# Kernel optimization log

Hardware: AMD Instinct MI355X
Metric: run time of the kernel (lower is better)

## Reference

```python
import jax, jax.numpy as jnp
import numpy as np

N_HEADS = 16
D_EMBED = 1024
D_HEAD = D_EMBED // N_HEADS  # 64
B, S = 2, 2048


def setup_inputs() -> dict:
    key = jax.random.key(0)
    ks = jax.random.split(key, 6)
    k = jax.random.normal(ks[0], (B, S, D_EMBED), dtype=jnp.float32)
    q = jax.random.normal(ks[1], (B, S, D_EMBED), dtype=jnp.float32)
    v = jax.random.normal(ks[2], (B, S, D_EMBED), dtype=jnp.float32)
    # per-head projections, shared across heads (nn.Linear(d_head, d_head, bias=False))
    scale = 1.0 / np.sqrt(D_HEAD)
    Wk = jax.random.normal(ks[3], (D_HEAD, D_HEAD), dtype=jnp.float32) * scale
    Wq = jax.random.normal(ks[4], (D_HEAD, D_HEAD), dtype=jnp.float32) * scale
    Wv = jax.random.normal(ks[5], (D_HEAD, D_HEAD), dtype=jnp.float32) * scale
    return {"k": k, "q": q, "v": v, "Wk": Wk, "Wq": Wq, "Wv": Wv}


def reference(k, q, v, Wk, Wq, Wv):
    b, s, _ = k.shape
    # split heads: [b, s, h, dh]
    kh = k.reshape(b, s, N_HEADS, D_HEAD)
    qh = q.reshape(b, s, N_HEADS, D_HEAD)
    vh = v.reshape(b, s, N_HEADS, D_HEAD)
    # shared per-head linear projection (y = x @ W^T, torch Linear convention)
    kh = jnp.einsum('bshd,ed->bshe', kh, Wk)
    qh = jnp.einsum('bshd,ed->bshe', qh, Wq)
    vh = jnp.einsum('bshd,ed->bshe', vh, Wv)
    # attention scores [b, h, q, k]
    scores = jnp.einsum('bqhd,bkhd->bhqk', qh, kh) / np.sqrt(D_HEAD).astype(np.float32)
    attn = jax.nn.softmax(scores, axis=-1)
    out = jnp.einsum('bhqk,bkhd->bqhd', attn, vh)
    return out.reshape(b, s, D_EMBED)
```

## Files before the change

kernel.cpp:

```cpp
#include <hip/hip_runtime.h>
#include <hip/hip_bf16.h>

typedef unsigned short u16;
typedef __bf16 bf16x8 __attribute__((ext_vector_type(8)));
typedef float f32x4 __attribute__((ext_vector_type(4)));

#define S_LEN 2048
#define NH 16
#define NB 2
#define HEAD_ELEMS (NB * NH * S_LEN * 64)

#if __has_builtin(__builtin_amdgcn_exp2f)
#define EXP2(x) __builtin_amdgcn_exp2f(x)
#else
#define EXP2(x) exp2f(x)
#endif

#define QSCALE 0.180336880f
#define SHIFT2 30.0f

__device__ __forceinline__ bf16x8 pack8(float4 a, float4 b, float sc) {
    union { bf16x8 v; __hip_bfloat162 h[4]; } r;
    r.h[0] = __float22bfloat162_rn(make_float2(a.x * sc, a.y * sc));
    r.h[1] = __float22bfloat162_rn(make_float2(a.z * sc, a.w * sc));
    r.h[2] = __float22bfloat162_rn(make_float2(b.x * sc, b.y * sc));
    r.h[3] = __float22bfloat162_rn(make_float2(b.z * sc, b.w * sc));
    return r.v;
}

__global__ __launch_bounds__(256) void proj_kq(
    const float* __restrict__ kin, const float* __restrict__ qin,
    const float* __restrict__ Wk, const float* __restrict__ Wq,
    u16* __restrict__ Kh, u16* __restrict__ Qh)
{
    __shared__ __align__(16) u16 Yld[8 * 16 * 72];

    const int tid = threadIdx.x;
    const int wave = tid >> 6;
    const int lane = tid & 63;
    const int quad = lane >> 4;
    const int l15 = lane & 15;
    const int stile = blockIdx.x;
    const int p = blockIdx.y;
    const int hh = blockIdx.z;
    const long row0 = (long)stile * 16;
    const int b = (int)(row0 >> 11);
    const int s0 = (int)(row0 & 2047);

    const float* X = p ? qin : kin;
    const float* W = p ? Wq : Wk;
    const float sc = p ? QSCALE : 1.0f;

    const float* xr0 = X + (row0 + l15) * 1024 + (hh * 8 + wave * 2) * 64 + quad * 8;
    const float* xr1 = xr0 + 64;
    float4 xa[4], xb[4];
    xa[0] = *(const float4*)(xr0);      xa[1] = *(const float4*)(xr0 + 4);
    xa[2] = *(const float4*)(xr0 + 32); xa[3] = *(const float4*)(xr0 + 36);
    xb[0] = *(const float4*)(xr1);      xb[1] = *(const float4*)(xr1 + 4);
    xb[2] = *(const float4*)(xr1 + 32); xb[3] = *(const float4*)(xr1 + 36);

    bf16x8 wf[4][2];
    #pragma unroll
    for (int nt = 0; nt < 4; ++nt) {
        const float* wr = W + (nt * 16 + l15) * 64 + quad * 8;
        wf[nt][0] = pack8(*(const float4*)(wr),      *(const float4*)(wr + 4),  sc);
        wf[nt][1] = pack8(*(const float4*)(wr + 32), *(const float4*)(wr + 36), sc);
    }

    #pragma unroll
    for (int hp = 0; hp < 2; ++hp) {
        const int hl = wave * 2 + hp;
        bf16x8 a0 = pack8(hp ? xb[0] : xa[0], hp ? xb[1] : xa[1], 1.0f);
        bf16x8 a1 = pack8(hp ? xb[2] : xa[2], hp ? xb[3] : xa[3], 1.0f);
        #pragma unroll
        for (int nt = 0; nt < 4; ++nt) {
            f32x4 c = (f32x4){0.f, 0.f, 0.f, 0.f};
            c = __builtin_amdgcn_mfma_f32_16x16x32_bf16(a0, wf[nt][0], c, 0, 0, 0);
            c = __builtin_amdgcn_mfma_f32_16x16x32_bf16(a1, wf[nt][1], c, 0, 0, 0);
            union { __hip_bfloat162 h2; u16 u[2]; } x01, x23;
            x01.h2 = __float22bfloat162_rn(make_float2(c[0], c[1]));
            x23.h2 = __float22bfloat162_rn(make_float2(c[2], c[3]));
            int base = (hl * 16 + quad * 4) * 72 + nt * 16 + l15;
            Yld[base]       = x01.u[0];
            Yld[base + 72]  = x01.u[1];
            Yld[base + 144] = x23.u[0];
            Yld[base + 216] = x23.u[1];
        }
    }
    __syncthreads();

    u16* dst = p ? Qh : Kh;
    #pragma unroll
    for (int it = 0; it < 4; ++it) {
        int idx = tid + it * 256;
        int eg = idx & 7, s = (idx >> 3) & 15, hl = idx >> 7;
        int bh = b * NH + hh * 8 + hl;
        *(float4*)(dst + ((long)bh * S_LEN + s0 + s) * 64 + eg * 8) =
            *(const float4*)&Yld[(hl * 16 + s) * 72 + eg * 8];
    }
}

__global__ __launch_bounds__(256) void proj_v(
    const float* __restrict__ vin, const float* __restrict__ Wv, u16* __restrict__ Vt)
{
    __shared__ __align__(16) u16 Vtile[64 * 72];

    const int tid = threadIdx.x;
    const int wave = tid >> 6;
    const int lane = tid & 63;
    const int quad = lane >> 4;
    const int l15 = lane & 15;
    const long row0 = (long)blockIdx.x * 64;
    const int b = (int)(row0 >> 11);
    const int s0 = (int)(row0 & 2047);
    const int h = blockIdx.y;
    const int bh = b * NH + h;

    const float* xr = vin + (row0 + wave * 16 + l15) * 1024 + h * 64 + quad * 8;
    float4 x4[4];
    x4[0] = *(const float4*)(xr);      x4[1] = *(const float4*)(xr + 4);
    x4[2] = *(const float4*)(xr + 32); x4[3] = *(const float4*)(xr + 36);

    bf16x8 wf[4][2];
    #pragma unroll
    for (int dt = 0; dt < 4; ++dt) {
        const float* wr = Wv + (dt * 16 + l15) * 64 + quad * 8;
        wf[dt][0] = pack8(*(const float4*)(wr),      *(const float4*)(wr + 4),  1.0f);
        wf[dt][1] = pack8(*(const float4*)(wr + 32), *(const float4*)(wr + 36), 1.0f);
    }

    bf16x8 x0 = pack8(x4[0], x4[1], 1.0f);
    bf16x8 x1 = pack8(x4[2], x4[3], 1.0f);

    #pragma unroll
    for (int dt = 0; dt < 4; ++dt) {
        f32x4 c = (f32x4){0.f, 0.f, 0.f, 0.f};
        c = __builtin_amdgcn_mfma_f32_16x16x32_bf16(wf[dt][0], x0, c, 0, 0, 0);
        c = __builtin_amdgcn_mfma_f32_16x16x32_bf16(wf[dt][1], x1, c, 0, 0, 0);
        int base = (dt * 16 + quad * 4) * 72 + wave * 16 + l15;
        union { __hip_bfloat162 h2; u16 u[2]; } x01, x23;
        x01.h2 = __float22bfloat162_rn(make_float2(c[0], c[1]));
        x23.h2 = __float22bfloat162_rn(make_float2(c[2], c[3]));
        Vtile[base]       = x01.u[0];
        Vtile[base + 72]  = x01.u[1];
        Vtile[base + 144] = x23.u[0];
        Vtile[base + 216] = x23.u[1];
    }
    __syncthreads();

    u16* dst = Vt + (long)bh * 64 * S_LEN + s0;
    #pragma unroll
    for (int it = 0; it < 2; ++it) {
        int idx = tid + it * 256;
        int sg = idx & 7, e = idx >> 3;
        *(float4*)(dst + (long)e * S_LEN + sg * 8) = *(const float4*)&Vtile[e * 72 + sg * 8];
    }
}

__global__ __launch_bounds__(256, 2) void attn_kernel(
    const u16* __restrict__ Qh, const u16* __restrict__ Kh,
    const u16* __restrict__ Vt, float* __restrict__ out)
{
    __shared__ __align__(16) u16 Qld[64 * 72];
    __shared__ __align__(16) float Old[4][64 * 20];
    __shared__ float lbc[4][64];

    const int tid = threadIdx.x;
    const int wave = tid >> 6;
    const int lane = tid & 63;
    const int quad = lane >> 4;
    const int l15 = lane & 15;
    const int qb = blockIdx.x;
    const int bh = blockIdx.y;
    const int b = bh >> 4, h = bh & 15;
    const int q0 = qb * 64;
    const u16* kb = Kh + (long)bh * S_LEN * 64;
    const u16* vb = Vt + (long)bh * 64 * S_LEN;

    {
        const u16* qp = Qh + ((long)bh * S_LEN + q0) * 64;
        #pragma unroll
        for (int i = 0; i < 2; ++i) {
            int idx = tid + i * 256;
            int row = idx >> 3, gg = idx & 7;
            *(float4*)&Qld[row * 72 + gg * 8] = *(const float4*)(qp + row * 64 + gg * 8);
        }
    }
    __syncthreads();

    const int krow_off = ((l15 >> 2) * 8 + (l15 & 3)) * 64;

    f32x4 oacc[4][4];
    #pragma unroll
    for (int g = 0; g < 4; ++g)
        #pragma unroll
        for (int dt = 0; dt < 4; ++dt) oacc[g][dt] = (f32x4){0.f, 0.f, 0.f, 0.f};
    float rs[4] = {0.f, 0.f, 0.f, 0.f};

    for (int kt = wave; kt < S_LEN / 64; kt += 4) {
        const u16* kt_p = kb + (long)kt * 4096;
        const u16* vt_p = vb + kt * 64;
        #pragma unroll
        for (int c = 0; c < 2; ++c) {
            bf16x8 kf[2][2], vf[4];
            #pragma unroll
            for (int nn = 0; nn < 2; ++nn) {
                const u16* kr = kt_p + c * 2048 + krow_off + nn * 256 + quad * 8;
                kf[nn][0] = *(const bf16x8*)(kr);
                kf[nn][1] = *(const bf16x8*)(kr + 32);
            }
            #pragma unroll
            for (int dt = 0; dt < 4; ++dt)
                vf[dt] = *(const bf16x8*)(vt_p + (long)(dt * 16 + l15) * S_LEN + c * 32 + quad * 8);

            #pragma unroll
            for (int g = 0; g < 4; ++g) {
                const u16* qrow = &Qld[(g * 16 + l15) * 72 + quad * 8];
                bf16x8 qb0 = *(const bf16x8*)(qrow);
                bf16x8 qb1 = *(const bf16x8*)(qrow + 32);
                f32x4 s0 = (f32x4){0.f, 0.f, 0.f, 0.f};
                f32x4 s1 = (f32x4){0.f, 0.f, 0.f, 0.f};
                s0 = __builtin_amdgcn_mfma_f32_16x16x32_bf16(kf[0][0], qb0, s0, 0, 0, 0);
                s0 = __builtin_amdgcn_mfma_f32_16x16x32_bf16(kf[0][1], qb1, s0, 0, 0, 0);
                s1 = __builtin_amdgcn_mfma_f32_16x16x32_bf16(kf[1][0], qb0, s1, 0, 0, 0);
                s1 = __builtin_amdgcn_mfma_f32_16x16x32_bf16(kf[1][1], qb1, s1, 0, 0, 0);

                float p00 = EXP2(s0[0] - SHIFT2), p01 = EXP2(s0[1] - SHIFT2);
                float p02 = EXP2(s0[2] - SHIFT2), p03 = EXP2(s0[3] - SHIFT2);
                float p10 = EXP2(s1[0] - SHIFT2), p11 = EXP2(s1[1] - SHIFT2);
                float p12 = EXP2(s1[2] - SHIFT2), p13 = EXP2(s1[3] - SHIFT2);
                rs[g] += ((p00 + p01) + (p02 + p03)) + ((p10 + p11) + (p12 + p13));

                union { bf16x8 v; __hip_bfloat162 h2[4]; } pf;
                pf.h2[0] = __float22bfloat162_rn(make_float2(p00, p01));
                pf.h2[1] = __float22bfloat162_rn(make_float2(p02, p03));
                pf.h2[2] = __float22bfloat162_rn(make_float2(p10, p11));
                pf.h2[3] = __float22bfloat162_rn(make_float2(p12, p13));

                #pragma unroll
                for (int dt = 0; dt < 4; ++dt)
                    oacc[g][dt] = __builtin_amdgcn_mfma_f32_16x16x32_bf16(vf[dt], pf.v, oacc[g][dt], 0, 0, 0);
            }
        }
    }

    #pragma unroll
    for (int g = 0; g < 4; ++g) {
        rs[g] += __shfl_xor(rs[g], 16);
        rs[g] += __shfl_xor(rs[g], 32);
    }
    if (lane < 16) {
        #pragma unroll
        for (int g = 0; g < 4; ++g) lbc[wave][g * 16 + lane] = rs[g];
    }
    __syncthreads();

    const int rq = tid >> 2, seg = tid & 3;
    const float linv = 1.0f / (lbc[0][rq] + lbc[1][rq] + lbc[2][rq] + lbc[3][rq]);
    float* op = out + ((long)(b * S_LEN + q0 + rq)) * 1024 + h * 64;

    #pragma unroll
    for (int ph = 0; ph < 4; ++ph) {
        #pragma unroll
        for (int g = 0; g < 4; ++g)
            *(f32x4*)&Old[wave][(g * 16 + l15) * 20 + quad * 4] = oacc[g][ph];
        __syncthreads();
        f32x4 a = (f32x4){0.f, 0.f, 0.f, 0.f};
        #pragma unroll
        for (int w = 0; w < 4; ++w) a += *(const f32x4*)&Old[w][rq * 20 + seg * 4];
        *(float4*)(op + ph * 16 + seg * 4) =
            make_float4(a[0] * linv, a[1] * linv, a[2] * linv, a[3] * linv);
        __syncthreads();
    }
}

extern "C" void kernel_launch(void* const* d_in, const int* in_sizes, int n_in,
                              void* d_out, int out_size, void* d_ws, size_t ws_size,
                              hipStream_t stream) {
    const float* kin = (const float*)d_in[0];
    const float* qin = (const float*)d_in[1];
    const float* vin = (const float*)d_in[2];
    const float* Wk  = (const float*)d_in[3];
    const float* Wq  = (const float*)d_in[4];
    const float* Wv  = (const float*)d_in[5];
    float* out = (float*)d_out;

    u16* wsp = (u16*)d_ws;
    u16* Kh = wsp;
    u16* Qh = wsp + (long)HEAD_ELEMS;
    u16* Vt = wsp + 2 * (long)HEAD_ELEMS;

    dim3 kqg(256, 2, 2);
    proj_kq<<<kqg, 256, 0, stream>>>(kin, qin, Wk, Wq, Kh, Qh);
    dim3 vg(64, 16);
    proj_v<<<vg, 256, 0, stream>>>(vin, Wv, Vt);
    dim3 g(S_LEN / 64, NB * NH);
    attn_kernel<<<g, 256, 0, stream>>>(Qh, Kh, Vt, out);
}
```

Baseline: 177.2 us.

## Keep Q in registers and double-buffer K/V register loads with MFMA priority

Q fragments now load straight from global memory into registers instead of being staged through shared memory, which removes the LDS tile and a block barrier. The K/V loop becomes a software pipeline with two register buffers, so the next half-tile's global loads are issued before computing on the current one, hiding load latency. The score shift is folded into the MFMA accumulator's initial value, and s_setprio raises wave priority around the MFMA sections. The cost is higher register pressure from holding Q and two K/V buffers, which could spill or limit occupancy under launch_bounds(256,2). The last iteration issues a redundant reload of the final tile.

```diff
diff --git a/kernel.cpp b/kernel.cpp
--- a/kernel.cpp
+++ b/kernel.cpp
@@ -161,12 +161,11 @@
     const u16* __restrict__ Qh, const u16* __restrict__ Kh,
     const u16* __restrict__ Vt, float* __restrict__ out)
 {
-    __shared__ __align__(16) u16 Qld[64 * 72];
     __shared__ __align__(16) float Old[4][64 * 20];
     __shared__ float lbc[4][64];
 
     const int tid = threadIdx.x;
-    const int wave = tid >> 6;
+    const int wave = __builtin_amdgcn_readfirstlane(tid >> 6);
     const int lane = tid & 63;
     const int quad = lane >> 4;
     const int l15 = lane & 15;
@@ -177,18 +176,18 @@
     const u16* kb = Kh + (long)bh * S_LEN * 64;
     const u16* vb = Vt + (long)bh * 64 * S_LEN;
 
+    const int koff = ((l15 >> 2) * 8 + (l15 & 3)) * 64 + quad * 8;
+    const int voff = l15 * S_LEN + quad * 8;
+
+    bf16x8 qf[4][2];
     {
-        const u16* qp = Qh + ((long)bh * S_LEN + q0) * 64;
-        #pragma unroll
-        for (int i = 0; i < 2; ++i) {
-            int idx = tid + i * 256;
-            int row = idx >> 3, gg = idx & 7;
-            *(float4*)&Qld[row * 72 + gg * 8] = *(const float4*)(qp + row * 64 + gg * 8);
+        const u16* qp = Qh + ((long)bh * S_LEN + q0 + l15) * 64 + quad * 8;
+        #pragma unroll
+        for (int g = 0; g < 4; ++g) {
+            qf[g][0] = *(const bf16x8*)(qp + g * 16 * 64);
+            qf[g][1] = *(const bf16x8*)(qp + g * 16 * 64 + 32);
         }
     }
-    __syncthreads();
-
-    const int krow_off = ((l15 >> 2) * 8 + (l15 & 3)) * 64;
 
     f32x4 oacc[4][4];
     #pragma unroll
@@ -197,51 +196,65 @@
         for (int dt = 0; dt < 4; ++dt) oacc[g][dt] = (f32x4){0.f, 0.f, 0.f, 0.f};
     float rs[4] = {0.f, 0.f, 0.f, 0.f};
 
-    for (int kt = wave; kt < S_LEN / 64; kt += 4) {
-        const u16* kt_p = kb + (long)kt * 4096;
-        const u16* vt_p = vb + kt * 64;
-        #pragma unroll
-        for (int c = 0; c < 2; ++c) {
-            bf16x8 kf[2][2], vf[4];
-            #pragma unroll
-            for (int nn = 0; nn < 2; ++nn) {
-                const u16* kr = kt_p + c * 2048 + krow_off + nn * 256 + quad * 8;
-                kf[nn][0] = *(const bf16x8*)(kr);
-                kf[nn][1] = *(const bf16x8*)(kr + 32);
-            }
+    auto loadKV = [&](const u16* kp, const u16* vp,
+                      bf16x8 (&kf)[2][2], bf16x8 (&vf)[4]) {
+        #pragma unroll
+        for (int nn = 0; nn < 2; ++nn) {
+            const u16* kr = kp + koff + nn * 256;
+            kf[nn][0] = *(const bf16x8*)(kr);
+            kf[nn][1] = *(const bf16x8*)(kr + 32);
+        }
+        #pragma unroll
+        for (int dt = 0; dt < 4; ++dt)
+            vf[dt] = *(const bf16x8*)(vp + voff + dt * 16 * S_LEN);
+    };
+
+    auto compute = [&](const bf16x8 (&kf)[2][2], const bf16x8 (&vf)[4]) {
+        #pragma unroll
+        for (int g = 0; g < 4; ++g) {
+            f32x4 s0 = (f32x4){-SHIFT2, -SHIFT2, -SHIFT2, -SHIFT2};
+            f32x4 s1 = (f32x4){-SHIFT2, -SHIFT2, -SHIFT2, -SHIFT2};
+            __builtin_amdgcn_s_setprio(1);
+            s0 = __builtin_amdgcn_mfma_f32_16x16x32_bf16(kf[0][0], qf[g][0], s0, 0, 0, 0);
+            s0 = __builtin_amdgcn_mfma_f32_16x16x32_bf16(kf[0][1], qf[g][1], s0, 0, 0, 0);
+            s1 = __builtin_amdgcn_mfma_f32_16x16x32_bf16(kf[1][0], qf[g][0], s1, 0, 0, 0);
+            s1 = __builtin_amdgcn_mfma_f32_16x16x32_bf16(kf[1][1], qf[g][1], s1, 0, 0, 0);
+            __builtin_amdgcn_s_setprio(0);
+
+            float p00 = EXP2(s0[0]), p01 = EXP2(s0[1]);
+            float p02 = EXP2(s0[2]), p03 = EXP2(s0[3]);
+            float p10 = EXP2(s1[0]), p11 = EXP2(s1[1]);
+            float p12 = EXP2(s1[2]), p13 = EXP2(s1[3]);
+            rs[g] += ((p00 + p01) + (p02 + p03)) + ((p10 + p11) + (p12 + p13));
+
+            union { bf16x8 v; __hip_bfloat162 h2[4]; } pf;
+            pf.h2[0] = __float22bfloat162_rn(make_float2(p00, p01));
+            pf.h2[1] = __float22bfloat162_rn(make_float2(p02, p03));
+            pf.h2[2] = __float22bfloat162_rn(make_float2(p10, p11));
+            pf.h2[3] = __float22bfloat162_rn(make_float2(p12, p13));
+
+            __builtin_amdgcn_s_setprio(1);
             #pragma unroll
             for (int dt = 0; dt < 4; ++dt)
-                vf[dt] = *(const bf16x8*)(vt_p + (long)(dt * 16 + l15) * S_LEN + c * 32 + quad * 8);
-
-            #pragma unroll
-            for (int g = 0; g < 4; ++g) {
-                const u16* qrow = &Qld[(g * 16 + l15) * 72 + quad * 8];
-                bf16x8 qb0 = *(const bf16x8*)(qrow);
-                bf16x8 qb1 = *(const bf16x8*)(qrow + 32);
-                f32x4 s0 = (f32x4){0.f, 0.f, 0.f, 0.f};
-                f32x4 s1 = (f32x4){0.f, 0.f, 0.f, 0.f};
-                s0 = __builtin_amdgcn_mfma_f32_16x16x32_bf16(kf[0][0], qb0, s0, 0, 0, 0);
-                s0 = __builtin_amdgcn_mfma_f32_16x16x32_bf16(kf[0][1], qb1, s0, 0, 0, 0);
-                s1 = __builtin_amdgcn_mfma_f32_16x16x32_bf16(kf[1][0], qb0, s1, 0, 0, 0);
-                s1 = __builtin_amdgcn_mfma_f32_16x16x32_bf16(kf[1][1], qb1, s1, 0, 0, 0);
-
-                float p00 = EXP2(s0[0] - SHIFT2), p01 = EXP2(s0[1] - SHIFT2);
-                float p02 = EXP2(s0[2] - SHIFT2), p03 = EXP2(s0[3] - SHIFT2);
-                float p10 = EXP2(s1[0] - SHIFT2), p11 = EXP2(s1[1] - SHIFT2);
-                float p12 = EXP2(s1[2] - SHIFT2), p13 = EXP2(s1[3] - SHIFT2);
-                rs[g] += ((p00 + p01) + (p02 + p03)) + ((p10 + p11) + (p12 + p13));
-
-                union { bf16x8 v; __hip_bfloat162 h2[4]; } pf;
-                pf.h2[0] = __float22bfloat162_rn(make_float2(p00, p01));
-                pf.h2[1] = __float22bfloat162_rn(make_float2(p02, p03));
-                pf.h2[2] = __float22bfloat162_rn(make_float2(p10, p11));
-                pf.h2[3] = __float22bfloat162_rn(make_float2(p12, p13));
-
-                #pragma unroll
-                for (int dt = 0; dt < 4; ++dt)
-                    oacc[g][dt] = __builtin_amdgcn_mfma_f32_16x16x32_bf16(vf[dt], pf.v, oacc[g][dt], 0, 0, 0);
-            }
+                oacc[g][dt] = __builtin_amdgcn_mfma_f32_16x16x32_bf16(vf[dt], pf.v, oacc[g][dt], 0, 0, 0);
+            __builtin_amdgcn_s_setprio(0);
         }
+    };
+
+    bf16x8 kfA[2][2], vfA[4], kfB[2][2], vfB[4];
+    const u16* kp = kb + wave * 4096;
+    const u16* vp = vb + wave * 64;
+    loadKV(kp, vp, kfA, vfA);
+
+    #pragma unroll 1
+    for (int kt = wave; kt < S_LEN / 64; kt += 4) {
+        loadKV(kp + 2048, vp + 32, kfB, vfB);
+        compute(kfA, vfA);
+        const u16* nkp = (kt < S_LEN / 64 - 4) ? kp + 4 * 4096 : kp;
+        const u16* nvp = (kt < S_LEN / 64 - 4) ? vp + 4 * 64   : vp;
+        loadKV(nkp, nvp, kfA, vfA);
+        compute(kfB, vfB);
+        kp = nkp; vp = nvp;
     }
 
     #pragma unroll
```

Measured after the change: 182.5 us. +3.0%, slower.

## Fuse K/Q/V projections into one launch and pre-swizzle K/V into fragment order

Applied to the files above, without the earlier changes.

Merges the KQ and V projection kernels into a single 2048-block launch. It also writes K and V into the workspace in MFMA-fragment order, so each lane in the attention kernel loads its bf16x8 fragments with fully contiguous 16-byte accesses instead of strided row gathers. This is meant to cut one launch and make the attention kernel's K/V global loads coalesced. The cost is more complex index arithmetic in the projection stores and a layout shared across kernels that is harder to maintain.

```diff
diff --git a/kernel.cpp b/kernel.cpp
--- a/kernel.cpp
+++ b/kernel.cpp
@@ -9,6 +9,7 @@
 #define NH 16
 #define NB 2
 #define HEAD_ELEMS (NB * NH * S_LEN * 64)
+#define BH_ELEMS (S_LEN * 64)
 
 #if __has_builtin(__builtin_amdgcn_exp2f)
 #define EXP2(x) __builtin_amdgcn_exp2f(x)
@@ -28,10 +29,12 @@
     return r.v;
 }
 
-__global__ __launch_bounds__(256) void proj_kq(
+__global__ __launch_bounds__(256) void proj_fused(
     const float* __restrict__ kin, const float* __restrict__ qin,
+    const float* __restrict__ vin,
     const float* __restrict__ Wk, const float* __restrict__ Wq,
-    u16* __restrict__ Kh, u16* __restrict__ Qh)
+    const float* __restrict__ Wv,
+    u16* __restrict__ Kh, u16* __restrict__ Qh, u16* __restrict__ Vt)
 {
     __shared__ __align__(16) u16 Yld[8 * 16 * 72];
 
@@ -40,120 +43,134 @@
     const int lane = tid & 63;
     const int quad = lane >> 4;
     const int l15 = lane & 15;
-    const int stile = blockIdx.x;
-    const int p = blockIdx.y;
-    const int hh = blockIdx.z;
-    const long row0 = (long)stile * 16;
-    const int b = (int)(row0 >> 11);
-    const int s0 = (int)(row0 & 2047);
-
-    const float* X = p ? qin : kin;
-    const float* W = p ? Wq : Wk;
-    const float sc = p ? QSCALE : 1.0f;
-
-    const float* xr0 = X + (row0 + l15) * 1024 + (hh * 8 + wave * 2) * 64 + quad * 8;
-    const float* xr1 = xr0 + 64;
-    float4 xa[4], xb[4];
-    xa[0] = *(const float4*)(xr0);      xa[1] = *(const float4*)(xr0 + 4);
-    xa[2] = *(const float4*)(xr0 + 32); xa[3] = *(const float4*)(xr0 + 36);
-    xb[0] = *(const float4*)(xr1);      xb[1] = *(const float4*)(xr1 + 4);
-    xb[2] = *(const float4*)(xr1 + 32); xb[3] = *(const float4*)(xr1 + 36);
-
-    bf16x8 wf[4][2];
-    #pragma unroll
-    for (int nt = 0; nt < 4; ++nt) {
-        const float* wr = W + (nt * 16 + l15) * 64 + quad * 8;
-        wf[nt][0] = pack8(*(const float4*)(wr),      *(const float4*)(wr + 4),  sc);
-        wf[nt][1] = pack8(*(const float4*)(wr + 32), *(const float4*)(wr + 36), sc);
-    }
-
-    #pragma unroll
-    for (int hp = 0; hp < 2; ++hp) {
-        const int hl = wave * 2 + hp;
-        bf16x8 a0 = pack8(hp ? xb[0] : xa[0], hp ? xb[1] : xa[1], 1.0f);
-        bf16x8 a1 = pack8(hp ? xb[2] : xa[2], hp ? xb[3] : xa[3], 1.0f);
+    const int bid = blockIdx.x;
+
+    if (bid < 1024) {
+        const int stile = bid & 255;
+        const int p = (bid >> 8) & 1;
+        const int hh = bid >> 9;
+        const long row0 = (long)stile * 16;
+        const int b = (int)(row0 >> 11);
+        const int s0 = (int)(row0 & 2047);
+
+        const float* X = p ? qin : kin;
+        const float* W = p ? Wq : Wk;
+        const float sc = p ? QSCALE : 1.0f;
+
+        const float* xr0 = X + (row0 + l15) * 1024 + (hh * 8 + wave * 2) * 64 + quad * 8;
+        const float* xr1 = xr0 + 64;
+        float4 xa[4], xb[4];
+        xa[0] = *(const float4*)(xr0);      xa[1] = *(const float4*)(xr0 + 4);
+        xa[2] = *(const float4*)(xr0 + 32); xa[3] = *(const float4*)(xr0 + 36);
+        xb[0] = *(const float4*)(xr1);      xb[1] = *(const float4*)(xr1 + 4);
+        xb[2] = *(const float4*)(xr1 + 32); xb[3] = *(const float4*)(xr1 + 36);
+
+        bf16x8 wf[4][2];
         #pragma unroll
         for (int nt = 0; nt < 4; ++nt) {
+            const float* wr = W + (nt * 16 + l15) * 64 + quad * 8;
+            wf[nt][0] = pack8(*(const float4*)(wr),      *(const float4*)(wr + 4),  sc);
+            wf[nt][1] = pack8(*(const float4*)(wr + 32), *(const float4*)(wr + 36), sc);
+        }
+
+        #pragma unroll
+        for (int hp = 0; hp < 2; ++hp) {
+            const int hl = wave * 2 + hp;
+            bf16x8 a0 = pack8(hp ? xb[0] : xa[0], hp ? xb[1] : xa[1], 1.0f);
+            bf16x8 a1 = pack8(hp ? xb[2] : xa[2], hp ? xb[3] : xa[3], 1.0f);
+            #pragma unroll
+            for (int nt = 0; nt < 4; ++nt) {
+                f32x4 c = (f32x4){0.f, 0.f, 0.f, 0.f};
+                c = __builtin_amdgcn_mfma_f32_16x16x32_bf16(a0, wf[nt][0], c, 0, 0, 0);
+                c = __builtin_amdgcn_mfma_f32_16x16x32_bf16(a1, wf[nt][1], c, 0, 0, 0);
+                union { __hip_bfloat162 h2; u16 u[2]; } x01, x23;
+                x01.h2 = __float22bfloat162_rn(make_float2(c[0], c[1]));
+                x23.h2 = __float22bfloat162_rn(make_float2(c[2], c[3]));
+                int base = (hl * 16 + quad * 4) * 72 + nt * 16 + l15;
+                Yld[base]       = x01.u[0];
+                Yld[base + 72]  = x01.u[1];
+                Yld[base + 144] = x23.u[0];
+                Yld[base + 216] = x23.u[1];
+            }
+        }
+        __syncthreads();
+
+        if (p) {
+            #pragma unroll
+            for (int it = 0; it < 4; ++it) {
+                int idx = tid + it * 256;
+                int eg = idx & 7, s = (idx >> 3) & 15, hl = idx >> 7;
+                int bh = b * NH + hh * 8 + hl;
+                *(float4*)(Qh + ((long)bh * S_LEN + s0 + s) * 64 + eg * 8) =
+                    *(const float4*)&Yld[(hl * 16 + s) * 72 + eg * 8];
+            }
+        } else {
+            #pragma unroll
+            for (int it = 0; it < 4; ++it) {
+                int idx = tid + it * 256;
+                int eg = idx & 7, s = (idx >> 3) & 15, hl = idx >> 7;
+                int bh = b * NH + hh * 8 + hl;
+                int sg = s0 + s;
+                int kt = sg >> 6, c = (sg >> 5) & 1, rp = sg & 31;
+                int nn = (rp >> 2) & 1;
+                int l15p = ((rp >> 3) << 2) | (rp & 3);
+                int j = eg >> 2, qd = eg & 3;
+                long off = (long)bh * BH_ELEMS
+                         + (long)((((kt * 2 + c) * 2 + nn) * 2 + j) * 512 + (qd * 16 + l15p) * 8);
+                *(float4*)(Kh + off) = *(const float4*)&Yld[(hl * 16 + s) * 72 + eg * 8];
+            }
+        }
+    } else {
+        const int vid = bid - 1024;
+        const long row0 = (long)(vid & 63) * 64;
+        const int b = (int)(row0 >> 11);
+        const int s0 = (int)(row0 & 2047);
+        const int h = vid >> 6;
+        const int bh = b * NH + h;
+        const int kt = s0 >> 6;
+
+        const float* xr = vin + (row0 + wave * 16 + l15) * 1024 + h * 64 + quad * 8;
+        float4 x4[4];
+        x4[0] = *(const float4*)(xr);      x4[1] = *(const float4*)(xr + 4);
+        x4[2] = *(const float4*)(xr + 32); x4[3] = *(const float4*)(xr + 36);
+
+        bf16x8 wf[4][2];
+        #pragma unroll
+        for (int dt = 0; dt < 4; ++dt) {
+            const float* wr = Wv + (dt * 16 + l15) * 64 + quad * 8;
+            wf[dt][0] = pack8(*(const float4*)(wr),      *(const float4*)(wr + 4),  1.0f);
+            wf[dt][1] = pack8(*(const float4*)(wr + 32), *(const float4*)(wr + 36), 1.0f);
+        }
+
+        bf16x8 x0 = pack8(x4[0], x4[1], 1.0f);
+        bf16x8 x1 = pack8(x4[2], x4[3], 1.0f);
+
+        #pragma unroll
+        for (int dt = 0; dt < 4; ++dt) {
             f32x4 c = (f32x4){0.f, 0.f, 0.f, 0.f};
-            c = __builtin_amdgcn_mfma_f32_16x16x32_bf16(a0, wf[nt][0], c, 0, 0, 0);
-            c = __builtin_amdgcn_mfma_f32_16x16x32_bf16(a1, wf[nt][1], c, 0, 0, 0);
+            c = __builtin_amdgcn_mfma_f32_16x16x32_bf16(wf[dt][0], x0, c, 0, 0, 0);
+            c = __builtin_amdgcn_mfma_f32_16x16x32_bf16(wf[dt][1], x1, c, 0, 0, 0);
+            int base = (dt * 16 + quad * 4) * 72 + wave * 16 + l15;
             union { __hip_bfloat162 h2; u16 u[2]; } x01, x23;
             x01.h2 = __float22bfloat162_rn(make_float2(c[0], c[1]));
             x23.h2 = __float22bfloat162_rn(make_float2(c[2], c[3]));
-            int base = (hl * 16 + quad * 4) * 72 + nt * 16 + l15;
             Yld[base]       = x01.u[0];
             Yld[base + 72]  = x01.u[1];
             Yld[base + 144] = x23.u[0];
             Yld[base + 216] = x23.u[1];
         }
-    }
-    __syncthreads();
-
-    u16* dst = p ? Qh : Kh;
-    #pragma unroll
-    for (int it = 0; it < 4; ++it) {
-        int idx = tid + it * 256;
-        int eg = idx & 7, s = (idx >> 3) & 15, hl = idx >> 7;
-        int bh = b * NH + hh * 8 + hl;
-        *(float4*)(dst + ((long)bh * S_LEN + s0 + s) * 64 + eg * 8) =
-            *(const float4*)&Yld[(hl * 16 + s) * 72 + eg * 8];
-    }
-}
-
-__global__ __launch_bounds__(256) void proj_v(
-    const float* __restrict__ vin, const float* __restrict__ Wv, u16* __restrict__ Vt)
-{
-    __shared__ __align__(16) u16 Vtile[64 * 72];
-
-    const int tid = threadIdx.x;
-    const int wave = tid >> 6;
-    const int lane = tid & 63;
-    const int quad = lane >> 4;
-    const int l15 = lane & 15;
-    const long row0 = (long)blockIdx.x * 64;
-    const int b = (int)(row0 >> 11);
-    const int s0 = (int)(row0 & 2047);
-    const int h = blockIdx.y;
-    const int bh = b * NH + h;
-
-    const float* xr = vin + (row0 + wave * 16 + l15) * 1024 + h * 64 + quad * 8;
-    float4 x4[4];
-    x4[0] = *(const float4*)(xr);      x4[1] = *(const float4*)(xr + 4);
-    x4[2] = *(const float4*)(xr + 32); x4[3] = *(const float4*)(xr + 36);
-
-    bf16x8 wf[4][2];
-    #pragma unroll
-    for (int dt = 0; dt < 4; ++dt) {
-        const float* wr = Wv + (dt * 16 + l15) * 64 + quad * 8;
-        wf[dt][0] = pack8(*(const float4*)(wr),      *(const float4*)(wr + 4),  1.0f);
-        wf[dt][1] = pack8(*(const float4*)(wr + 32), *(const float4*)(wr + 36), 1.0f);
-    }
-
-    bf16x8 x0 = pack8(x4[0], x4[1], 1.0f);
-    bf16x8 x1 = pack8(x4[2], x4[3], 1.0f);
-
-    #pragma unroll
-    for (int dt = 0; dt < 4; ++dt) {
-        f32x4 c = (f32x4){0.f, 0.f, 0.f, 0.f};
-        c = __builtin_amdgcn_mfma_f32_16x16x32_bf16(wf[dt][0], x0, c, 0, 0, 0);
-        c = __builtin_amdgcn_mfma_f32_16x16x32_bf16(wf[dt][1], x1, c, 0, 0, 0);
-        int base = (dt * 16 + quad * 4) * 72 + wave * 16 + l15;
-        union { __hip_bfloat162 h2; u16 u[2]; } x01, x23;
-        x01.h2 = __float22bfloat162_rn(make_float2(c[0], c[1]));
-        x23.h2 = __float22bfloat162_rn(make_float2(c[2], c[3]));
-        Vtile[base]       = x01.u[0];
-        Vtile[base + 72]  = x01.u[1];
-        Vtile[base + 144] = x23.u[0];
-        Vtile[base + 216] = x23.u[1];
-    }
-    __syncthreads();
-
-    u16* dst = Vt + (long)bh * 64 * S_LEN + s0;
-    #pragma unroll
-    for (int it = 0; it < 2; ++it) {
-        int idx = tid + it * 256;
-        int sg = idx & 7, e = idx >> 3;
-        *(float4*)(dst + (long)e * S_LEN + sg * 8) = *(const float4*)&Vtile[e * 72 + sg * 8];
+        __syncthreads();
+
+        u16* dstb = Vt + (long)bh * BH_ELEMS;
+        #pragma unroll
+        for (int it = 0; it < 2; ++it) {
+            int idx = tid + it * 256;
+            int sg = idx & 7, e_row = idx >> 3;
+            int c = sg >> 2, lhi = sg & 3;
+            int dt = e_row >> 4, l15p = e_row & 15;
+            long off = (long)(((kt * 2 + c) * 4 + dt) * 512 + (lhi * 16 + l15p) * 8);
+            *(float4*)(dstb + off) = *(const float4*)&Yld[e_row * 72 + sg * 8];
+        }
     }
 }
 
@@ -174,8 +191,8 @@
     const int bh = blockIdx.y;
     const int b = bh >> 4, h = bh & 15;
     const int q0 = qb * 64;
-    const u16* kb = Kh + (long)bh * S_LEN * 64;
-    const u16* vb = Vt + (long)bh * 64 * S_LEN;
+    const u16* kb = Kh + (long)bh * BH_ELEMS + lane * 8;
+    const u16* vb = Vt + (long)bh * BH_ELEMS + lane * 8;
 
     {
         const u16* qp = Qh + ((long)bh * S_LEN + q0) * 64;
@@ -188,8 +205,6 @@
     }
     __syncthreads();
 
-    const int krow_off = ((l15 >> 2) * 8 + (l15 & 3)) * 64;
-
     f32x4 oacc[4][4];
     #pragma unroll
     for (int g = 0; g < 4; ++g)
@@ -198,20 +213,18 @@
     float rs[4] = {0.f, 0.f, 0.f, 0.f};
 
     for (int kt = wave; kt < S_LEN / 64; kt += 4) {
-        const u16* kt_p = kb + (long)kt * 4096;
-        const u16* vt_p = vb + kt * 64;
+        const u16* kt_k = kb + kt * 4096;
+        const u16* kt_v = vb + kt * 4096;
         #pragma unroll
         for (int c = 0; c < 2; ++c) {
             bf16x8 kf[2][2], vf[4];
-            #pragma unroll
-            for (int nn = 0; nn < 2; ++nn) {
-                const u16* kr = kt_p + c * 2048 + krow_off + nn * 256 + quad * 8;
-                kf[nn][0] = *(const bf16x8*)(kr);
-                kf[nn][1] = *(const bf16x8*)(kr + 32);
-            }
+            kf[0][0] = *(const bf16x8*)(kt_k + c * 2048);
+            kf[0][1] = *(const bf16x8*)(kt_k + c * 2048 + 512);
+            kf[1][0] = *(const bf16x8*)(kt_k + c * 2048 + 1024);
+            kf[1][1] = *(const bf16x8*)(kt_k + c * 2048 + 1536);
             #pragma unroll
             for (int dt = 0; dt < 4; ++dt)
-                vf[dt] = *(const bf16x8*)(vt_p + (long)(dt * 16 + l15) * S_LEN + c * 32 + quad * 8);
+                vf[dt] = *(const bf16x8*)(kt_v + c * 2048 + dt * 512);
 
             #pragma unroll
             for (int g = 0; g < 4; ++g) {
@@ -290,10 +303,7 @@
     u16* Qh = wsp + (long)HEAD_ELEMS;
     u16* Vt = wsp + 2 * (long)HEAD_ELEMS;
 
-    dim3 kqg(256, 2, 2);
-    proj_kq<<<kqg, 256, 0, stream>>>(kin, qin, Wk, Wq, Kh, Qh);
-    dim3 vg(64, 16);
-    proj_v<<<vg, 256, 0, stream>>>(vin, Wv, Vt);
+    proj_fused<<<dim3(2048), 256, 0, stream>>>(kin, qin, vin, Wk, Wq, Wv, Kh, Qh, Vt);
     dim3 g(S_LEN / 64, NB * NH);
     attn_kernel<<<g, 256, 0, stream>>>(Qh, Kh, Vt, out);
 }
```

New measurement: 149.4 us. -15.7%, faster.
